# Kernel tuning notes

Measured on AMD Instinct MI355X. Metric: run time of the kernel, lower is better.

Reference implementation:

```python
import jax, jax.numpy as jnp
import numpy as np

NUM_CLASSES = 2
THRESHOLD = 0.35
NEGPOS_RATIO = 3
VAR0, VAR1 = 0.1, 0.2
ALPHA = 1.0
B, P, G = 16, 131072, 64


def _iou(a, b):
    # a: [G,4] point-form gts, b: [P,4] point-form priors -> [G,P]
    tl = jnp.maximum(a[:, None, :2], b[None, :, :2])
    br = jnp.minimum(a[:, None, 2:], b[None, :, 2:])
    wh = jnp.clip(br - tl, 0.0)
    inter = wh[..., 0] * wh[..., 1]
    area_a = (a[:, 2] - a[:, 0]) * (a[:, 3] - a[:, 1])
    area_b = (b[:, 2] - b[:, 0]) * (b[:, 3] - b[:, 1])
    return inter / (area_a[:, None] + area_b[None, :] - inter)


def setup_inputs() -> dict:
    key = jax.random.key(0)
    k1, k2, k3, k4, k5, k6 = jax.random.split(key, 6)
    loc_preds = jax.random.normal(k1, (B, P, 4), jnp.float32)
    cls_preds = jax.random.normal(k2, (B, P, NUM_CLASSES), jnp.float32)
    # priors in center form [cx, cy, w, h]
    pcxy = jax.random.uniform(k3, (P, 2), jnp.float32)
    pwh = 0.02 + 0.15 * jax.random.uniform(k4, (P, 2), jnp.float32)
    priorbox = jnp.concatenate([pcxy, pwh], axis=1)
    # ground-truth boxes; stored as [y1,x1,y2,x2,label] so that the module's
    # column permutation [1,0,3,2] yields valid point-form [x1,y1,x2,y2]
    xy1 = 0.8 * jax.random.uniform(k5, (B, G, 2), jnp.float32)
    wh = 0.02 + 0.1 * jax.random.uniform(k6, (B, G, 2), jnp.float32)
    xy2 = xy1 + wh
    boxes_perm = jnp.stack([xy1[..., 1], xy1[..., 0], xy2[..., 1], xy2[..., 0]], axis=-1)
    labels = jnp.ones((B, G, 1), jnp.float32)  # single foreground class (face)
    targets = jnp.concatenate([boxes_perm, labels], axis=-1)
    return {"loc_preds": loc_preds, "cls_preds": cls_preds,
            "priorbox": priorbox, "targets": targets}


def _loss(loc_preds, cls_preds, priorbox, targets):
    priors_c = priorbox[: loc_preds.shape[1], :]
    priors_pt = jnp.concatenate(
        [priors_c[:, :2] - priors_c[:, 2:] / 2,
         priors_c[:, :2] + priors_c[:, 2:] / 2], axis=1)
    num_g = targets.shape[1]

    def match_one(t):
        gts = t[:, :4][:, jnp.array([1, 0, 3, 2])]  # -> point form [x1,y1,x2,y2]
        labels = t[:, 4]
        ov = _iou(gts, priors_pt)                    # [G,P]
        best_prior_idx = jnp.argmax(ov, axis=1)      # [G]
        bto = jnp.max(ov, axis=0)                    # [P] best gt overlap per prior
        bti = jnp.argmax(ov, axis=0)                 # [P]
        bto = bto.at[best_prior_idx].set(2.0)        # force best prior per gt
        bti = bti.at[best_prior_idx].set(jnp.arange(num_g))
        conf = jnp.where(bto < THRESHOLD, 0.0, labels[bti])
        m = gts[bti]                                 # [P,4] matched gt boxes
        g_cxcy = ((m[:, :2] + m[:, 2:]) / 2 - priors_c[:, :2]) / (VAR0 * priors_c[:, 2:])
        g_wh = jnp.log((m[:, 2:] - m[:, :2]) / priors_c[:, 2:]) / VAR1
        return conf, jnp.concatenate([g_cxcy, g_wh], axis=1)

    cls_batch, loc_batch = jax.vmap(match_one)(targets)
    cls_batch = jax.lax.stop_gradient(cls_batch)   # targets require no grad
    loc_batch = jax.lax.stop_gradient(loc_batch)

    pos = cls_batch > 0                              # [B,P]
    npos = jnp.sum(pos)

    # smooth-L1 over positive priors, mean over selected elements (size_average)
    d = loc_preds - loc_batch
    ad = jnp.abs(d)
    sl1 = jnp.where(ad < 1.0, 0.5 * d * d, ad - 0.5)
    loss_loc = jnp.sum(sl1 * pos[..., None]) / jnp.maximum(npos * 4, 1).astype(sl1.dtype)

    # per-prior CE loss for hard-negative mining
    ignore = cls_batch < 0
    lbl = jnp.where(ignore, 0.0, cls_batch).astype(jnp.int32)
    lse = jax.nn.logsumexp(cls_preds, axis=-1)       # [B,P]
    gathered = jnp.take_along_axis(cls_preds, lbl[..., None], axis=-1)[..., 0]
    loss_c = jnp.where(pos | ignore, 0.0, lse - gathered)
    # two-stage sort: rank of each prior by descending loss
    loss_idx = jnp.argsort(-loss_c, axis=1)
    idx_rank = jnp.argsort(loss_idx, axis=1)
    num_pos_img = jnp.sum(pos, axis=1, keepdims=True)
    num_neg = jnp.minimum(NEGPOS_RATIO * num_pos_img, pos.shape[1] - 1)
    neg = idx_rank < num_neg
    mask = pos | neg
    # cross-entropy over mined samples, mean over selected (size_average)
    loss_cls = jnp.sum((lse - gathered) * mask) / jnp.maximum(jnp.sum(mask), 1).astype(lse.dtype)

    loss = (loss_cls + ALPHA * loss_loc) / npos.astype(lse.dtype)
    return loss, loss_loc, loss_cls


def reference(loc_preds, cls_preds, priorbox, targets):
    return _loss(loc_preds, cls_preds, priorbox, targets)
```

## Files before the change

kernel.cpp:

```cpp
#include <hip/hip_runtime.h>

#define BB 16
#define PP 131072
#define GG 64
#define THRESH 0.35f
#define RMAX 0.086f
#define NCHUNK 16
#define CPRIOR 8192

#define OFF_BESTP  0
#define OFF_H1C    131072
#define OFF_H1S    4325376
#define OFF_NPOSP  8519680
#define OFF_PCP    8520704
#define OFF_LOCP   8521728
#define OFF_CIDX   8522752
#define OFF_DONE   8522816
#define OFF_SELI   8522880
#define OFF_RESN   8523136
#define OFF_RESK   8523200
#define OFF_RESC   8523264
#define OFF_RESL   8523328
#define OFF_KEYS   8523392
#define OFF_BTO    16912000
#define OFF_BTI    25300608
#define OFF_CAND   27397760

__global__ __launch_bounds__(1024) void k_match(
    const float* __restrict__ priorbox, const float* __restrict__ targets,
    unsigned long long* __restrict__ bestp, float* __restrict__ bto,
    unsigned char* __restrict__ bti)
{
    __shared__ unsigned mlo[4096], mhi[4096];
    __shared__ float4 gxy[GG];
    __shared__ float gar[GG];
    __shared__ unsigned long long sbest[GG];
    const int b = blockIdx.y, chunk = blockIdx.x, tid = threadIdx.x;

    for (int i = tid; i < 4096; i += 1024) { mlo[i] = 0u; mhi[i] = 0u; }
    if (tid < GG) {
        const float* t = targets + (size_t)(b * GG + tid) * 5;
        float x1 = t[1], y1 = t[0], x2 = t[3], y2 = t[2];
        gxy[tid] = make_float4(x1, y1, x2, y2);
        gar[tid] = (x2 - x1) * (y2 - y1);
        sbest[tid] = 0ull;
    }
    __syncthreads();

    {
        const int g = tid & 63, strip = tid >> 6;
        float4 a = gxy[g];
        float ex1 = a.x - RMAX, ey1 = a.y - RMAX;
        float ex2 = a.z + RMAX, ey2 = a.w + RMAX;
        int cx0 = max(0, (int)(ex1 * 64.f));
        int cx1 = min(63, (int)ceilf(ex2 * 64.f) - 1);
        int cy0 = max(0, (int)(ey1 * 64.f));
        int cy1 = min(63, (int)ceilf(ey2 * 64.f) - 1);
        unsigned bit = 1u << (g & 31);
        unsigned* marr = (g < 32) ? mlo : mhi;
        for (int cy = cy0 + strip; cy <= cy1; cy += 16)
            for (int cx = cx0; cx <= cx1; cx++)
                atomicOr(&marr[cy * 64 + cx], bit);
    }
    __syncthreads();

#pragma unroll
    for (int j = 0; j < 8; j++) {
        const int p = chunk * CPRIOR + j * 1024 + tid;
        float4 pr = *reinterpret_cast<const float4*>(priorbox + (size_t)p * 4);
        float hx = 0.5f * pr.z, hy = 0.5f * pr.w;
        float px1 = pr.x - hx, py1 = pr.y - hy;
        float px2 = pr.x + hx, py2 = pr.y + hy;
        float par = (px2 - px1) * (py2 - py1);
        int cx = min(63, max(0, (int)(pr.x * 64.f)));
        int cy = min(63, max(0, (int)(pr.y * 64.f)));
        const int cell = cy * 64 + cx;
        unsigned m0 = mlo[cell], m1 = mhi[cell];
        const unsigned long long notp = (unsigned long long)(~(unsigned)p);
        float bv = -1.f; int bg = 0;
#pragma unroll 1
        for (int half = 0; half < 2; half++) {
            unsigned m = half ? m1 : m0;
            const int gbase = half ? 32 : 0;
            while (m) {
                const int g = gbase + __ffs(m) - 1;
                m &= m - 1;
                float4 a = gxy[g];
                float w = fminf(a.z, px2) - fmaxf(a.x, px1);
                float h = fminf(a.w, py2) - fmaxf(a.y, py1);
                w = fmaxf(w, 0.f); h = fmaxf(h, 0.f);
                float inter = w * h;
                float v = inter * __builtin_amdgcn_rcpf(gar[g] + par - inter);
                if (v > bv) { bv = v; bg = g; }
                if (v > 0.f) {
                    unsigned long long pk =
                        (((unsigned long long)__float_as_uint(v)) << 32) | notp;
                    atomicMax(&sbest[g], pk);
                }
            }
        }
        bto[(size_t)b * PP + p] = bv;
        bti[(size_t)b * PP + p] = (unsigned char)bg;
    }

    __syncthreads();
    if (tid < GG) bestp[(b * NCHUNK + chunk) * GG + tid] = sbest[tid];
}

__global__ __launch_bounds__(1024) void k_loss(
    const float* __restrict__ loc_preds, const float* __restrict__ cls_preds,
    const float* __restrict__ priorbox, const float* __restrict__ targets,
    const unsigned long long* __restrict__ bestp,
    const float* __restrict__ bto, const unsigned char* __restrict__ bti,
    unsigned* __restrict__ keys, unsigned* __restrict__ h1c, float* __restrict__ h1s,
    int* __restrict__ nposp, float* __restrict__ pcp, float* __restrict__ locp,
    unsigned* __restrict__ cidx, unsigned* __restrict__ done)
{
    __shared__ unsigned long long tmp64[1024];
    __shared__ unsigned hcnt[4096];
    __shared__ float hsum[4096];
    __shared__ float gx1[GG], gy1[GG], gx2[GG], gy2[GG], glab[GG];
    __shared__ unsigned blist[GG];
    __shared__ int nb;
    __shared__ float sred[32];
    __shared__ int sredi[16];
    const int b = blockIdx.y, chunk = blockIdx.x, tid = threadIdx.x;

    if (tid == 0 && chunk == 0) { cidx[b] = 0u; if (b == 0) *done = 0u; }

    tmp64[tid] = bestp[(b * NCHUNK + (tid >> 6)) * GG + (tid & 63)];
    for (int i = tid; i < 4096; i += 1024) { hcnt[i] = 0u; hsum[i] = 0.f; }
    if (tid < GG) {
        const float* t = targets + (size_t)(b * GG + tid) * 5;
        gx1[tid] = t[1]; gy1[tid] = t[0]; gx2[tid] = t[3]; gy2[tid] = t[2];
        glab[tid] = t[4];
    }
    __syncthreads();
    if (tid < GG) {
        unsigned long long m = tmp64[tid];
        for (int c = 1; c < NCHUNK; c++) {
            unsigned long long v = tmp64[c * GG + tid];
            m = v > m ? v : m;
        }
        tmp64[tid] = m;
    }
    __syncthreads();
    if (tid == 0) {
        int n = 0;
        for (int g = 0; g < GG; g++) {
            unsigned long long m = tmp64[g];
            if (m) {
                unsigned p = ~((unsigned)(m & 0xFFFFFFFFull));
                if ((int)(p >> 13) == chunk) blist[n++] = ((p & 8191u) << 6) | (unsigned)g;
            }
        }
        nb = n;
    }
    __syncthreads();

    const int nbl = nb;
    float locpart = 0.f, clspart = 0.f; int cnt = 0;
#pragma unroll
    for (int j = 0; j < 8; j++) {
        const int plocal = j * 1024 + tid;
        const size_t ip = (size_t)b * PP + chunk * CPRIOR + plocal;
        const float bv = bto[ip];
        int g = bti[ip];
        bool isb = false;
        for (int i = 0; i < nbl; i++) {
            unsigned e = blist[i];
            if ((int)(e >> 6) == plocal) { isb = true; g = (int)(e & 63u); }
        }
        const float2 cl = *reinterpret_cast<const float2*>(cls_preds + ip * 2);
        const float mx = fmaxf(cl.x, cl.y);
        const float lse = mx + log1pf(expf(fminf(cl.x, cl.y) - mx));
        const float conf = isb ? glab[g] : ((bv < THRESH) ? 0.f : glab[g]);
        unsigned key = 0u;
        if (conf > 0.f) {
            float gathered = (((int)conf) == 0) ? cl.x : cl.y;
            clspart += lse - gathered;
            cnt++;
            const int p = chunk * CPRIOR + plocal;
            float4 pr = *reinterpret_cast<const float4*>(priorbox + (size_t)p * 4);
            float mx1 = gx1[g], my1 = gy1[g], mx2 = gx2[g], my2 = gy2[g];
            float gcx = ((mx1 + mx2) * 0.5f - pr.x) / (0.1f * pr.z);
            float gcy = ((my1 + my2) * 0.5f - pr.y) / (0.1f * pr.w);
            float gw = logf((mx2 - mx1) / pr.z) / 0.2f;
            float gh = logf((my2 - my1) / pr.w) / 0.2f;
            float4 lp = *reinterpret_cast<const float4*>(loc_preds + ip * 4);
            float d0 = lp.x - gcx, d1 = lp.y - gcy, d2 = lp.z - gw, d3 = lp.w - gh;
            float a0 = fabsf(d0), a1 = fabsf(d1), a2 = fabsf(d2), a3 = fabsf(d3);
            locpart += ((a0 < 1.f) ? 0.5f * d0 * d0 : a0 - 0.5f)
                     + ((a1 < 1.f) ? 0.5f * d1 * d1 : a1 - 0.5f)
                     + ((a2 < 1.f) ? 0.5f * d2 * d2 : a2 - 0.5f)
                     + ((a3 < 1.f) ? 0.5f * d3 * d3 : a3 - 0.5f);
        } else {
            float lc = lse - cl.x;
            key = __float_as_uint(lc);
            atomicAdd(&hcnt[key >> 20], 1u);
            atomicAdd(&hsum[key >> 20], lc);
        }
        keys[ip] = key;
    }

    for (int o = 32; o; o >>= 1) {
        locpart += __shfl_xor(locpart, o);
        clspart += __shfl_xor(clspart, o);
        cnt     += __shfl_xor(cnt, o);
    }
    const int w = tid >> 6;
    if ((tid & 63) == 0) { sred[w] = locpart; sred[16 + w] = clspart; sredi[w] = cnt; }
    __syncthreads();
    if (tid == 0) {
        float l = 0.f, c = 0.f; int n = 0;
        for (int i = 0; i < 16; i++) { l += sred[i]; c += sred[16 + i]; n += sredi[i]; }
        nposp[b * NCHUNK + chunk] = n;
        pcp[b * NCHUNK + chunk] = c;
        locp[b * NCHUNK + chunk] = l;
    }
    __syncthreads();
    for (int i = tid; i < 4096; i += 1024) {
        h1c[(b * NCHUNK + chunk) * 4096 + i] = hcnt[i];
        h1s[(b * NCHUNK + chunk) * 4096 + i] = hsum[i];
    }
}

template <int NBINS>
__device__ void find_kth_par(const unsigned* __restrict__ h, int k, int* sel, int* krem)
{
    constexpr int PER = NBINS / 1024;
    __shared__ unsigned wsum_[16];
    __shared__ int res_[2];
    const int tid = threadIdx.x, lane = tid & 63, wid = tid >> 6;
    __syncthreads();
    unsigned own[PER];
    unsigned s = 0;
#pragma unroll
    for (int i = 0; i < PER; i++) { own[i] = h[NBINS - 1 - (tid * PER + i)]; s += own[i]; }
    unsigned incl = s;
    for (int d = 1; d < 64; d <<= 1) {
        unsigned t = __shfl_up(incl, d);
        if (lane >= d) incl += t;
    }
    if (lane == 63) wsum_[wid] = incl;
    if (tid == 0) { res_[0] = -1; res_[1] = 0; }
    __syncthreads();
    unsigned woff = 0;
    for (int w = 0; w < 16; w++) woff += (w < wid) ? wsum_[w] : 0u;
    const unsigned texcl = woff + incl - s;
    if (k > 0 && texcl < (unsigned)k && texcl + s >= (unsigned)k) {
        unsigned run = texcl;
#pragma unroll
        for (int i = 0; i < PER; i++) {
            run += own[i];
            if (run >= (unsigned)k) {
                res_[0] = NBINS - 1 - (tid * PER + i);
                res_[1] = k - (int)(run - own[i]);
                break;
            }
        }
    }
    __syncthreads();
    *sel = res_[0]; *krem = res_[1];
}

__device__ float block_sum_f(float v)
{
    __shared__ float rs[16];
    const int tid = threadIdx.x;
    __syncthreads();
    for (int o = 32; o; o >>= 1) v += __shfl_xor(v, o);
    if ((tid & 63) == 0) rs[tid >> 6] = v;
    __syncthreads();
    float s = 0.f;
    for (int i = 0; i < 16; i++) s += rs[i];
    return s;
}

__global__ __launch_bounds__(1024) void k_compact(
    const unsigned* __restrict__ keys, const unsigned* __restrict__ h1c,
    const int* __restrict__ nposp, unsigned* __restrict__ cand,
    unsigned* __restrict__ cidx, int* __restrict__ seli)
{
    __shared__ unsigned h1tot[4096];
    __shared__ int snp;
    __shared__ unsigned wcnt[16], wbase[16];
    __shared__ unsigned bbase;
    const int b = blockIdx.y, chunk = blockIdx.x, tid = threadIdx.x;
    const int lane = tid & 63, wid = tid >> 6;
    if (tid == 0) {
        int np = 0;
        for (int c = 0; c < NCHUNK; c++) np += nposp[b * NCHUNK + c];
        snp = np;
    }
    for (int i = tid; i < 4096; i += 1024) {
        unsigned s = 0;
        for (int c = 0; c < NCHUNK; c++) s += h1c[(b * NCHUNK + c) * 4096 + i];
        h1tot[i] = s;
    }
    unsigned kv[8];
#pragma unroll
    for (int j = 0; j < 8; j++)
        kv[j] = keys[(size_t)b * PP + chunk * CPRIOR + j * 1024 + tid];
    __syncthreads();
    const int np = snp;
    const int k = min(3 * np, PP - 1);
    int sel1, kk1;
    find_kth_par<4096>(h1tot, k, &sel1, &kk1);
    if (chunk == 0 && tid == 0) {
        seli[b * 4 + 0] = sel1; seli[b * 4 + 1] = kk1;
        seli[b * 4 + 2] = np;   seli[b * 4 + 3] = k;
    }
    const unsigned s1 = (unsigned)sel1;

    unsigned long long mv[8];
    unsigned wn = 0;
#pragma unroll
    for (int j = 0; j < 8; j++) {
        mv[j] = __ballot((kv[j] >> 20) == s1);
        wn += (unsigned)__popcll(mv[j]);
    }
    if (lane == 0) wcnt[wid] = wn;
    __syncthreads();
    if (tid == 0) {
        unsigned run = 0;
        for (int w = 0; w < 16; w++) { wbase[w] = run; run += wcnt[w]; }
        bbase = run ? atomicAdd(&cidx[b], run) : 0u;
    }
    __syncthreads();
    unsigned run = bbase + wbase[wid];
    const unsigned long long lanemask = (1ull << lane) - 1ull;
#pragma unroll
    for (int j = 0; j < 8; j++) {
        if ((kv[j] >> 20) == s1)
            cand[(size_t)b * PP + run + (unsigned)__popcll(mv[j] & lanemask)] = kv[j];
        run += (unsigned)__popcll(mv[j]);
    }
}

__global__ __launch_bounds__(1024) void k_select(
    const unsigned* __restrict__ cand, const unsigned* __restrict__ cidx,
    const float* __restrict__ h1s, const int* __restrict__ seli,
    const float* __restrict__ pcp, const float* __restrict__ locp,
    int* __restrict__ resn, int* __restrict__ resk,
    float* __restrict__ resc, float* __restrict__ resl,
    unsigned* __restrict__ done, float* __restrict__ out)
{
    __shared__ unsigned ch[1024];
    __shared__ float cs[1024];
    __shared__ int lastflag;
    const int b = blockIdx.x, tid = threadIdx.x;
    const int sel1 = seli[b * 4 + 0], kk1 = seli[b * 4 + 1];
    const int np   = seli[b * 4 + 2], k   = seli[b * 4 + 3];
    const unsigned ncand = cidx[b];

    float nh = 0.f;
    for (int i = tid * 4; i < tid * 4 + 4; i++) {
        if (i > sel1) {
            for (int c = 0; c < NCHUNK; c++) nh += h1s[(b * NCHUNK + c) * 4096 + i];
        }
    }
    float negsum_high = block_sum_f(nh);

    ch[tid] = 0u; cs[tid] = 0.f;
    __syncthreads();
    for (unsigned i = tid; i < ncand; i += 1024) {
        unsigned v = cand[(size_t)b * PP + i];
        unsigned bin = (v >> 10) & 1023u;
        atomicAdd(&ch[bin], 1u);
        atomicAdd(&cs[bin], __uint_as_float(v));
    }
    __syncthreads();
    int sel2, kk2;
    find_kth_par<1024>(ch, (sel1 < 0) ? 0 : kk1, &sel2, &kk2);
    float sumhi2 = block_sum_f((sel2 >= 0 && tid > sel2) ? cs[tid] : 0.f);

    __syncthreads();
    ch[tid] = 0u; cs[tid] = 0.f;
    __syncthreads();
    if (sel2 >= 0) {
        for (unsigned i = tid; i < ncand; i += 1024) {
            unsigned v = cand[(size_t)b * PP + i];
            if (((v >> 10) & 1023u) == (unsigned)sel2) {
                atomicAdd(&ch[v & 1023u], 1u);
                atomicAdd(&cs[v & 1023u], __uint_as_float(v));
            }
        }
    }
    __syncthreads();
    int sel3, needeq;
    find_kth_par<1024>(ch, (sel2 < 0) ? 0 : kk2, &sel3, &needeq);
    float sumhi3 = block_sum_f((sel3 >= 0 && tid > sel3) ? cs[tid] : 0.f);

    if (tid == 0) {
        float pcsum = 0.f, locsum = 0.f;
        for (int c = 0; c < NCHUNK; c++) {
            pcsum += pcp[b * NCHUNK + c];
            locsum += locp[b * NCHUNK + c];
        }
        float add = 0.f;
        if (sel3 >= 0 && needeq > 0) {
            unsigned Kstar = ((unsigned)sel1 << 20) | ((unsigned)sel2 << 10) | (unsigned)sel3;
            add = needeq * __uint_as_float(Kstar);
        }
        resn[b] = np;
        resk[b] = k;
        resc[b] = pcsum + negsum_high + sumhi2 + sumhi3 + add;
        resl[b] = locsum;
        __threadfence();
        unsigned old = atomicAdd(done, 1u);
        lastflag = (old == BB - 1) ? 1 : 0;
    }
    __syncthreads();
    if (!lastflag || tid != 0) return;

    __threadfence();
    volatile int* vrn = (volatile int*)resn;
    volatile int* vrk = (volatile int*)resk;
    volatile float* vrc = (volatile float*)resc;
    volatile float* vrl = (volatile float*)resl;
    int npt = 0; long long maskc = 0; float clsnum = 0.f, locnum = 0.f;
    for (int b2 = 0; b2 < BB; b2++) {
        npt += vrn[b2];
        maskc += (long long)vrn[b2] + vrk[b2];
        clsnum += vrc[b2];
        locnum += vrl[b2];
    }
    float denom_loc = (float)((4 * npt > 1) ? 4 * npt : 1);
    float denom_cls = (float)((maskc > 1) ? maskc : 1);
    float loss_loc = locnum / denom_loc;
    float loss_cls = clsnum / denom_cls;
    out[0] = (loss_cls + loss_loc) / (float)npt;
    out[1] = loss_loc;
    out[2] = loss_cls;
}

extern "C" void kernel_launch(void* const* d_in, const int* in_sizes, int n_in,
                              void* d_out, int out_size, void* d_ws, size_t ws_size,
                              hipStream_t stream)
{
    const float* loc_preds = (const float*)d_in[0];
    const float* cls_preds = (const float*)d_in[1];
    const float* priorbox  = (const float*)d_in[2];
    const float* targets   = (const float*)d_in[3];
    float* out = (float*)d_out;

    char* ws = (char*)d_ws;
    unsigned long long* bestp = (unsigned long long*)(ws + OFF_BESTP);
    unsigned* h1c    = (unsigned*)(ws + OFF_H1C);
    float*    h1s    = (float*)(ws + OFF_H1S);
    int*      nposp  = (int*)(ws + OFF_NPOSP);
    float*    pcp    = (float*)(ws + OFF_PCP);
    float*    locp   = (float*)(ws + OFF_LOCP);
    unsigned* cidx   = (unsigned*)(ws + OFF_CIDX);
    unsigned* done   = (unsigned*)(ws + OFF_DONE);
    int*      seli   = (int*)(ws + OFF_SELI);
    int*      resn   = (int*)(ws + OFF_RESN);
    int*      resk   = (int*)(ws + OFF_RESK);
    float*    resc   = (float*)(ws + OFF_RESC);
    float*    resl   = (float*)(ws + OFF_RESL);
    unsigned* keys   = (unsigned*)(ws + OFF_KEYS);
    float*    bto    = (float*)(ws + OFF_BTO);
    unsigned char* bti = (unsigned char*)(ws + OFF_BTI);
    unsigned* cand   = (unsigned*)(ws + OFF_CAND);

    k_match<<<dim3(NCHUNK, BB), 1024, 0, stream>>>(priorbox, targets, bestp, bto, bti);
    k_loss<<<dim3(NCHUNK, BB), 1024, 0, stream>>>(loc_preds, cls_preds, priorbox, targets,
                                                  bestp, bto, bti, keys, h1c, h1s,
                                                  nposp, pcp, locp, cidx, done);
    k_compact<<<dim3(NCHUNK, BB), 1024, 0, stream>>>(keys, h1c, nposp, cand, cidx, seli);
    k_select<<<BB, 1024, 0, stream>>>(cand, cidx, h1s, seli, pcp, locp,
                                      resn, resk, resc, resl, done, out);
}
```

Before: 113.2 us.

## Pack match results into bytes and reduce partials with global atomics

The match kernel now writes one byte per prior that holds the best-gt index plus a positive-threshold flag, replacing the separate float overlap and byte index arrays. Per-chunk partial buffers for best priors, histograms and sums are replaced by global atomic accumulation, with a new init kernel that zeroes them. This removes the serial multi-chunk reductions in the compact and select kernels. Grids for match and loss are doubled to 32 chunks, and the IoU loop handles two gts per iteration. The trade is more atomic traffic and float-atomic ordering nondeterminism in the sums.

```diff
diff --git a/kernel.cpp b/kernel.cpp
--- a/kernel.cpp
+++ b/kernel.cpp
@@ -5,44 +5,57 @@
 #define GG 64
 #define THRESH 0.35f
 #define RMAX 0.086f
-#define NCHUNK 16
-#define CPRIOR 8192
-
-#define OFF_BESTP  0
-#define OFF_H1C    131072
-#define OFF_H1S    4325376
-#define OFF_NPOSP  8519680
-#define OFF_PCP    8520704
-#define OFF_LOCP   8521728
-#define OFF_CIDX   8522752
-#define OFF_DONE   8522816
-#define OFF_SELI   8522880
-#define OFF_RESN   8523136
-#define OFF_RESK   8523200
-#define OFF_RESC   8523264
-#define OFF_RESL   8523328
-#define OFF_KEYS   8523392
-#define OFF_BTO    16912000
-#define OFF_BTI    25300608
-#define OFF_CAND   27397760
-
-__global__ __launch_bounds__(1024) void k_match(
+#define NCH 32
+#define CPR 4096
+#define NCC 16
+#define CPC 8192
+
+#define OFF_BESTG   0
+#define OFF_H1TOT   8192
+#define OFF_H1STOT  270336
+#define OFF_NPOSI   532480
+#define OFF_PCI     532544
+#define OFF_LOCI    532608
+#define OFF_CIDX    532672
+#define OFF_DONE    532736
+#define OFF_SELI    532800
+#define OFF_RESN    533056
+#define OFF_RESK    533120
+#define OFF_RESC    533184
+#define OFF_RESL    533248
+#define OFF_PU8     533312
+#define OFF_KEYS    2630464
+#define OFF_CAND    11019072
+
+__global__ __launch_bounds__(1024) void k_init(
+    unsigned* __restrict__ bestg32, int* __restrict__ nposi, float* __restrict__ pci,
+    float* __restrict__ loci, unsigned* __restrict__ cidx, unsigned* __restrict__ done)
+{
+    const int t = threadIdx.x;
+    bestg32[t] = 0u; bestg32[t + 1024] = 0u;
+    if (t < BB) { nposi[t] = 0; pci[t] = 0.f; loci[t] = 0.f; cidx[t] = 0u; }
+    if (t == BB) *done = 0u;
+}
+
+__global__ __launch_bounds__(1024, 8) void k_match(
     const float* __restrict__ priorbox, const float* __restrict__ targets,
-    unsigned long long* __restrict__ bestp, float* __restrict__ bto,
-    unsigned char* __restrict__ bti)
-{
-    __shared__ unsigned mlo[4096], mhi[4096];
+    unsigned long long* __restrict__ bestg, unsigned char* __restrict__ pu8,
+    unsigned* __restrict__ h1tot, float* __restrict__ h1stot)
+{
+    __shared__ unsigned msk[8192];
     __shared__ float4 gxy[GG];
-    __shared__ float gar[GG];
     __shared__ unsigned long long sbest[GG];
     const int b = blockIdx.y, chunk = blockIdx.x, tid = threadIdx.x;
 
-    for (int i = tid; i < 4096; i += 1024) { mlo[i] = 0u; mhi[i] = 0u; }
+    {
+        const int zb = (b * NCH + chunk) * 128;
+        if (tid < 128) h1tot[zb + tid] = 0u;
+        else if (tid < 256) h1stot[zb + tid - 128] = 0.f;
+    }
+    for (int i = tid; i < 8192; i += 1024) msk[i] = 0u;
     if (tid < GG) {
         const float* t = targets + (size_t)(b * GG + tid) * 5;
-        float x1 = t[1], y1 = t[0], x2 = t[3], y2 = t[2];
-        gxy[tid] = make_float4(x1, y1, x2, y2);
-        gar[tid] = (x2 - x1) * (y2 - y1);
+        gxy[tid] = make_float4(t[1], t[0], t[3], t[2]);
         sbest[tid] = 0ull;
     }
     __syncthreads();
@@ -50,23 +63,21 @@
     {
         const int g = tid & 63, strip = tid >> 6;
         float4 a = gxy[g];
-        float ex1 = a.x - RMAX, ey1 = a.y - RMAX;
-        float ex2 = a.z + RMAX, ey2 = a.w + RMAX;
-        int cx0 = max(0, (int)(ex1 * 64.f));
-        int cx1 = min(63, (int)ceilf(ex2 * 64.f) - 1);
-        int cy0 = max(0, (int)(ey1 * 64.f));
-        int cy1 = min(63, (int)ceilf(ey2 * 64.f) - 1);
+        int cx0 = max(0, (int)((a.x - RMAX) * 64.f));
+        int cx1 = min(63, (int)ceilf((a.z + RMAX) * 64.f) - 1);
+        int cy0 = max(0, (int)((a.y - RMAX) * 64.f));
+        int cy1 = min(63, (int)ceilf((a.w + RMAX) * 64.f) - 1);
         unsigned bit = 1u << (g & 31);
-        unsigned* marr = (g < 32) ? mlo : mhi;
+        const int word = (g >> 5);
         for (int cy = cy0 + strip; cy <= cy1; cy += 16)
             for (int cx = cx0; cx <= cx1; cx++)
-                atomicOr(&marr[cy * 64 + cx], bit);
-    }
-    __syncthreads();
-
-#pragma unroll
-    for (int j = 0; j < 8; j++) {
-        const int p = chunk * CPRIOR + j * 1024 + tid;
+                atomicOr(&msk[2 * (cy * 64 + cx) + word], bit);
+    }
+    __syncthreads();
+
+#pragma unroll
+    for (int j = 0; j < 4; j++) {
+        const int p = chunk * CPR + j * 1024 + tid;
         float4 pr = *reinterpret_cast<const float4*>(priorbox + (size_t)p * 4);
         float hx = 0.5f * pr.z, hy = 0.5f * pr.w;
         float px1 = pr.x - hx, py1 = pr.y - hy;
@@ -74,84 +85,78 @@
         float par = (px2 - px1) * (py2 - py1);
         int cx = min(63, max(0, (int)(pr.x * 64.f)));
         int cy = min(63, max(0, (int)(pr.y * 64.f)));
-        const int cell = cy * 64 + cx;
-        unsigned m0 = mlo[cell], m1 = mhi[cell];
+        uint2 mm = *reinterpret_cast<uint2*>(&msk[2 * (cy * 64 + cx)]);
+        unsigned long long m = ((unsigned long long)mm.y << 32) | mm.x;
         const unsigned long long notp = (unsigned long long)(~(unsigned)p);
         float bv = -1.f; int bg = 0;
-#pragma unroll 1
-        for (int half = 0; half < 2; half++) {
-            unsigned m = half ? m1 : m0;
-            const int gbase = half ? 32 : 0;
-            while (m) {
-                const int g = gbase + __ffs(m) - 1;
-                m &= m - 1;
-                float4 a = gxy[g];
-                float w = fminf(a.z, px2) - fmaxf(a.x, px1);
-                float h = fminf(a.w, py2) - fmaxf(a.y, py1);
-                w = fmaxf(w, 0.f); h = fmaxf(h, 0.f);
-                float inter = w * h;
-                float v = inter * __builtin_amdgcn_rcpf(gar[g] + par - inter);
-                if (v > bv) { bv = v; bg = g; }
-                if (v > 0.f) {
-                    unsigned long long pk =
-                        (((unsigned long long)__float_as_uint(v)) << 32) | notp;
-                    atomicMax(&sbest[g], pk);
-                }
-            }
-        }
-        bto[(size_t)b * PP + p] = bv;
-        bti[(size_t)b * PP + p] = (unsigned char)bg;
-    }
-
-    __syncthreads();
-    if (tid < GG) bestp[(b * NCHUNK + chunk) * GG + tid] = sbest[tid];
-}
-
-__global__ __launch_bounds__(1024) void k_loss(
+        while (m) {
+            const int g0 = __ffsll(m) - 1; m &= m - 1;
+            const bool has1 = (m != 0ull);
+            const int g1 = has1 ? (__ffsll(m) - 1) : g0;
+            if (has1) m &= m - 1;
+            float4 a0 = gxy[g0];
+            float4 a1 = gxy[g1];
+            float w0 = fmaxf(fminf(a0.z, px2) - fmaxf(a0.x, px1), 0.f);
+            float h0 = fmaxf(fminf(a0.w, py2) - fmaxf(a0.y, py1), 0.f);
+            float w1 = fmaxf(fminf(a1.z, px2) - fmaxf(a1.x, px1), 0.f);
+            float h1 = fmaxf(fminf(a1.w, py2) - fmaxf(a1.y, py1), 0.f);
+            float ar0 = (a0.z - a0.x) * (a0.w - a0.y);
+            float ar1 = (a1.z - a1.x) * (a1.w - a1.y);
+            float i0 = w0 * h0, i1 = w1 * h1;
+            float v0 = i0 * __builtin_amdgcn_rcpf(ar0 + par - i0);
+            float v1 = i1 * __builtin_amdgcn_rcpf(ar1 + par - i1);
+            if (v0 > bv) { bv = v0; bg = g0; }
+            if (has1 && v1 > bv) { bv = v1; bg = g1; }
+            if (v0 > 0.f)
+                atomicMax(&sbest[g0],
+                          (((unsigned long long)__float_as_uint(v0)) << 32) | notp);
+            if (has1 && v1 > 0.f)
+                atomicMax(&sbest[g1],
+                          (((unsigned long long)__float_as_uint(v1)) << 32) | notp);
+        }
+        pu8[(size_t)b * PP + p] = (unsigned char)(bg | ((bv >= THRESH) ? 0x80 : 0));
+    }
+
+    __syncthreads();
+    if (tid < GG) {
+        unsigned long long s = sbest[tid];
+        if (s) atomicMax(&bestg[b * GG + tid], s);
+    }
+}
+
+__global__ __launch_bounds__(1024, 8) void k_loss(
     const float* __restrict__ loc_preds, const float* __restrict__ cls_preds,
     const float* __restrict__ priorbox, const float* __restrict__ targets,
-    const unsigned long long* __restrict__ bestp,
-    const float* __restrict__ bto, const unsigned char* __restrict__ bti,
-    unsigned* __restrict__ keys, unsigned* __restrict__ h1c, float* __restrict__ h1s,
-    int* __restrict__ nposp, float* __restrict__ pcp, float* __restrict__ locp,
-    unsigned* __restrict__ cidx, unsigned* __restrict__ done)
-{
-    __shared__ unsigned long long tmp64[1024];
+    const unsigned long long* __restrict__ bestg, const unsigned char* __restrict__ pu8,
+    unsigned* __restrict__ keys, unsigned* __restrict__ h1tot, float* __restrict__ h1stot,
+    int* __restrict__ nposi, float* __restrict__ pci, float* __restrict__ loci)
+{
     __shared__ unsigned hcnt[4096];
     __shared__ float hsum[4096];
-    __shared__ float gx1[GG], gy1[GG], gx2[GG], gy2[GG], glab[GG];
+    __shared__ float4 gxy[GG];
+    __shared__ float glab[GG];
     __shared__ unsigned blist[GG];
     __shared__ int nb;
     __shared__ float sred[32];
     __shared__ int sredi[16];
     const int b = blockIdx.y, chunk = blockIdx.x, tid = threadIdx.x;
-
-    if (tid == 0 && chunk == 0) { cidx[b] = 0u; if (b == 0) *done = 0u; }
-
-    tmp64[tid] = bestp[(b * NCHUNK + (tid >> 6)) * GG + (tid & 63)];
+    const int lane = tid & 63, wid = tid >> 6;
+
     for (int i = tid; i < 4096; i += 1024) { hcnt[i] = 0u; hsum[i] = 0.f; }
     if (tid < GG) {
         const float* t = targets + (size_t)(b * GG + tid) * 5;
-        gx1[tid] = t[1]; gy1[tid] = t[0]; gx2[tid] = t[3]; gy2[tid] = t[2];
+        gxy[tid] = make_float4(t[1], t[0], t[3], t[2]);
         glab[tid] = t[4];
-    }
-    __syncthreads();
-    if (tid < GG) {
-        unsigned long long m = tmp64[tid];
-        for (int c = 1; c < NCHUNK; c++) {
-            unsigned long long v = tmp64[c * GG + tid];
-            m = v > m ? v : m;
-        }
-        tmp64[tid] = m;
     }
     __syncthreads();
     if (tid == 0) {
         int n = 0;
         for (int g = 0; g < GG; g++) {
-            unsigned long long m = tmp64[g];
+            unsigned long long m = bestg[b * GG + g];
             if (m) {
                 unsigned p = ~((unsigned)(m & 0xFFFFFFFFull));
-                if ((int)(p >> 13) == chunk) blist[n++] = ((p & 8191u) << 6) | (unsigned)g;
+                if ((int)(p >> 12) == chunk)
+                    blist[n++] = (((p & (CPR - 1)) << 6) | (unsigned)g);
             }
         }
         nb = n;
@@ -161,32 +166,31 @@
     const int nbl = nb;
     float locpart = 0.f, clspart = 0.f; int cnt = 0;
 #pragma unroll
-    for (int j = 0; j < 8; j++) {
+    for (int j = 0; j < 4; j++) {
         const int plocal = j * 1024 + tid;
-        const size_t ip = (size_t)b * PP + chunk * CPRIOR + plocal;
-        const float bv = bto[ip];
-        int g = bti[ip];
-        bool isb = false;
+        const size_t ip = (size_t)b * PP + chunk * CPR + plocal;
+        const unsigned m8 = pu8[ip];
+        int g = m8 & 63;
+        bool pos = (m8 >> 7) != 0;
         for (int i = 0; i < nbl; i++) {
             unsigned e = blist[i];
-            if ((int)(e >> 6) == plocal) { isb = true; g = (int)(e & 63u); }
+            if ((int)(e >> 6) == plocal) { pos = true; g = (int)(e & 63u); }
         }
         const float2 cl = *reinterpret_cast<const float2*>(cls_preds + ip * 2);
         const float mx = fmaxf(cl.x, cl.y);
         const float lse = mx + log1pf(expf(fminf(cl.x, cl.y) - mx));
-        const float conf = isb ? glab[g] : ((bv < THRESH) ? 0.f : glab[g]);
         unsigned key = 0u;
-        if (conf > 0.f) {
-            float gathered = (((int)conf) == 0) ? cl.x : cl.y;
+        if (pos && glab[g] > 0.f) {
+            float gathered = (((int)glab[g]) == 0) ? cl.x : cl.y;
             clspart += lse - gathered;
             cnt++;
-            const int p = chunk * CPRIOR + plocal;
+            const int p = chunk * CPR + plocal;
             float4 pr = *reinterpret_cast<const float4*>(priorbox + (size_t)p * 4);
-            float mx1 = gx1[g], my1 = gy1[g], mx2 = gx2[g], my2 = gy2[g];
-            float gcx = ((mx1 + mx2) * 0.5f - pr.x) / (0.1f * pr.z);
-            float gcy = ((my1 + my2) * 0.5f - pr.y) / (0.1f * pr.w);
-            float gw = logf((mx2 - mx1) / pr.z) / 0.2f;
-            float gh = logf((my2 - my1) / pr.w) / 0.2f;
+            float4 gt = gxy[g];
+            float gcx = ((gt.x + gt.z) * 0.5f - pr.x) / (0.1f * pr.z);
+            float gcy = ((gt.y + gt.w) * 0.5f - pr.y) / (0.1f * pr.w);
+            float gw = logf((gt.z - gt.x) / pr.z) / 0.2f;
+            float gh = logf((gt.w - gt.y) / pr.w) / 0.2f;
             float4 lp = *reinterpret_cast<const float4*>(loc_preds + ip * 4);
             float d0 = lp.x - gcx, d1 = lp.y - gcy, d2 = lp.z - gw, d3 = lp.w - gh;
             float a0 = fabsf(d0), a1 = fabsf(d1), a2 = fabsf(d2), a3 = fabsf(d3);
@@ -208,20 +212,22 @@
         clspart += __shfl_xor(clspart, o);
         cnt     += __shfl_xor(cnt, o);
     }
-    const int w = tid >> 6;
-    if ((tid & 63) == 0) { sred[w] = locpart; sred[16 + w] = clspart; sredi[w] = cnt; }
+    if (lane == 0) { sred[wid] = locpart; sred[16 + wid] = clspart; sredi[wid] = cnt; }
     __syncthreads();
     if (tid == 0) {
         float l = 0.f, c = 0.f; int n = 0;
         for (int i = 0; i < 16; i++) { l += sred[i]; c += sred[16 + i]; n += sredi[i]; }
-        nposp[b * NCHUNK + chunk] = n;
-        pcp[b * NCHUNK + chunk] = c;
-        locp[b * NCHUNK + chunk] = l;
+        if (n)        atomicAdd(&nposi[b], n);
+        if (c != 0.f) atomicAdd(&pci[b], c);
+        if (l != 0.f) atomicAdd(&loci[b], l);
     }
     __syncthreads();
     for (int i = tid; i < 4096; i += 1024) {
-        h1c[(b * NCHUNK + chunk) * 4096 + i] = hcnt[i];
-        h1s[(b * NCHUNK + chunk) * 4096 + i] = hsum[i];
+        unsigned cc = hcnt[i];
+        if (cc) {
+            atomicAdd(&h1tot[b * 4096 + i], cc);
+            atomicAdd(&h1stot[b * 4096 + i], hsum[i]);
+        }
     }
 }
 
@@ -278,35 +284,24 @@
 }
 
 __global__ __launch_bounds__(1024) void k_compact(
-    const unsigned* __restrict__ keys, const unsigned* __restrict__ h1c,
-    const int* __restrict__ nposp, unsigned* __restrict__ cand,
+    const unsigned* __restrict__ keys, const unsigned* __restrict__ h1tot,
+    const int* __restrict__ nposi, unsigned* __restrict__ cand,
     unsigned* __restrict__ cidx, int* __restrict__ seli)
 {
-    __shared__ unsigned h1tot[4096];
-    __shared__ int snp;
     __shared__ unsigned wcnt[16], wbase[16];
     __shared__ unsigned bbase;
     const int b = blockIdx.y, chunk = blockIdx.x, tid = threadIdx.x;
     const int lane = tid & 63, wid = tid >> 6;
-    if (tid == 0) {
-        int np = 0;
-        for (int c = 0; c < NCHUNK; c++) np += nposp[b * NCHUNK + c];
-        snp = np;
-    }
-    for (int i = tid; i < 4096; i += 1024) {
-        unsigned s = 0;
-        for (int c = 0; c < NCHUNK; c++) s += h1c[(b * NCHUNK + c) * 4096 + i];
-        h1tot[i] = s;
-    }
+
     unsigned kv[8];
 #pragma unroll
     for (int j = 0; j < 8; j++)
-        kv[j] = keys[(size_t)b * PP + chunk * CPRIOR + j * 1024 + tid];
-    __syncthreads();
-    const int np = snp;
+        kv[j] = keys[(size_t)b * PP + chunk * CPC + j * 1024 + tid];
+
+    const int np = nposi[b];
     const int k = min(3 * np, PP - 1);
     int sel1, kk1;
-    find_kth_par<4096>(h1tot, k, &sel1, &kk1);
+    find_kth_par<4096>(h1tot + b * 4096, k, &sel1, &kk1);
     if (chunk == 0 && tid == 0) {
         seli[b * 4 + 0] = sel1; seli[b * 4 + 1] = kk1;
         seli[b * 4 + 2] = np;   seli[b * 4 + 3] = k;
@@ -340,8 +335,8 @@
 
 __global__ __launch_bounds__(1024) void k_select(
     const unsigned* __restrict__ cand, const unsigned* __restrict__ cidx,
-    const float* __restrict__ h1s, const int* __restrict__ seli,
-    const float* __restrict__ pcp, const float* __restrict__ locp,
+    const float* __restrict__ h1stot, const int* __restrict__ seli,
+    const float* __restrict__ pci, const float* __restrict__ loci,
     int* __restrict__ resn, int* __restrict__ resk,
     float* __restrict__ resc, float* __restrict__ resl,
     unsigned* __restrict__ done, float* __restrict__ out)
@@ -355,13 +350,11 @@
     const unsigned ncand = cidx[b];
 
     float nh = 0.f;
-    for (int i = tid * 4; i < tid * 4 + 4; i++) {
-        if (i > sel1) {
-            for (int c = 0; c < NCHUNK; c++) nh += h1s[(b * NCHUNK + c) * 4096 + i];
-        }
-    }
+    for (int i = tid; i < 4096; i += 1024)
+        if (i > sel1) nh += h1stot[b * 4096 + i];
     float negsum_high = block_sum_f(nh);
 
+    __syncthreads();
     ch[tid] = 0u; cs[tid] = 0.f;
     __syncthreads();
     for (unsigned i = tid; i < ncand; i += 1024) {
@@ -393,11 +386,6 @@
     float sumhi3 = block_sum_f((sel3 >= 0 && tid > sel3) ? cs[tid] : 0.f);
 
     if (tid == 0) {
-        float pcsum = 0.f, locsum = 0.f;
-        for (int c = 0; c < NCHUNK; c++) {
-            pcsum += pcp[b * NCHUNK + c];
-            locsum += locp[b * NCHUNK + c];
-        }
         float add = 0.f;
         if (sel3 >= 0 && needeq > 0) {
             unsigned Kstar = ((unsigned)sel1 << 20) | ((unsigned)sel2 << 10) | (unsigned)sel3;
@@ -405,8 +393,8 @@
         }
         resn[b] = np;
         resk[b] = k;
-        resc[b] = pcsum + negsum_high + sumhi2 + sumhi3 + add;
-        resl[b] = locsum;
+        resc[b] = pci[b] + negsum_high + sumhi2 + sumhi3 + add;
+        resl[b] = loci[b];
         __threadfence();
         unsigned old = atomicAdd(done, 1u);
         lastflag = (old == BB - 1) ? 1 : 0;
@@ -446,12 +434,12 @@
     float* out = (float*)d_out;
 
     char* ws = (char*)d_ws;
-    unsigned long long* bestp = (unsigned long long*)(ws + OFF_BESTP);
-    unsigned* h1c    = (unsigned*)(ws + OFF_H1C);
-    float*    h1s    = (float*)(ws + OFF_H1S);
-    int*      nposp  = (int*)(ws + OFF_NPOSP);
-    float*    pcp    = (float*)(ws + OFF_PCP);
-    float*    locp   = (float*)(ws + OFF_LOCP);
+    unsigned long long* bestg = (unsigned long long*)(ws + OFF_BESTG);
+    unsigned* h1tot  = (unsigned*)(ws + OFF_H1TOT);
+    float*    h1stot = (float*)(ws + OFF_H1STOT);
+    int*      nposi  = (int*)(ws + OFF_NPOSI);
+    float*    pci    = (float*)(ws + OFF_PCI);
+    float*    loci   = (float*)(ws + OFF_LOCI);
     unsigned* cidx   = (unsigned*)(ws + OFF_CIDX);
     unsigned* done   = (unsigned*)(ws + OFF_DONE);
     int*      seli   = (int*)(ws + OFF_SELI);
@@ -459,16 +447,17 @@
     int*      resk   = (int*)(ws + OFF_RESK);
     float*    resc   = (float*)(ws + OFF_RESC);
     float*    resl   = (float*)(ws + OFF_RESL);
+    unsigned char* pu8 = (unsigned char*)(ws + OFF_PU8);
     unsigned* keys   = (unsigned*)(ws + OFF_KEYS);
-    float*    bto    = (float*)(ws + OFF_BTO);
-    unsigned char* bti = (unsigned char*)(ws + OFF_BTI);
     unsigned* cand   = (unsigned*)(ws + OFF_CAND);
 
-    k_match<<<dim3(NCHUNK, BB), 1024, 0, stream>>>(priorbox, targets, bestp, bto, bti);
-    k_loss<<<dim3(NCHUNK, BB), 1024, 0, stream>>>(loc_preds, cls_preds, priorbox, targets,
-                                                  bestp, bto, bti, keys, h1c, h1s,
-                                                  nposp, pcp, locp, cidx, done);
-    k_compact<<<dim3(NCHUNK, BB), 1024, 0, stream>>>(keys, h1c, nposp, cand, cidx, seli);
-    k_select<<<BB, 1024, 0, stream>>>(cand, cidx, h1s, seli, pcp, locp,
+    k_init<<<1, 1024, 0, stream>>>((unsigned*)bestg, nposi, pci, loci, cidx, done);
+    k_match<<<dim3(NCH, BB), 1024, 0, stream>>>(priorbox, targets, bestg, pu8,
+                                                h1tot, h1stot);
+    k_loss<<<dim3(NCH, BB), 1024, 0, stream>>>(loc_preds, cls_preds, priorbox, targets,
+                                               bestg, pu8, keys, h1tot, h1stot,
+                                               nposi, pci, loci);
+    k_compact<<<dim3(NCC, BB), 1024, 0, stream>>>(keys, h1tot, nposi, cand, cidx, seli);
+    k_select<<<BB, 1024, 0, stream>>>(cand, cidx, h1stot, seli, pci, loci,
                                       resn, resk, resc, resl, done, out);
 }
```

Result: faster. 99.14 us (-12.5%).
